# Optimization experiments

Hardware: AMD Instinct MI355X
Metric: run time of the kernel (lower is better)

## Reference

```python
import jax, jax.numpy as jnp
import numpy as np

B, N, NH, F = 4, 4096, 16, 8      # batch, grid cells, input points per cell, raw features
D, FF, H, PE = 256, 1024, 8, 32   # model_dim, ff_dim, n_heads, pos_emb_dim
NG, NI = 8192, 65536              # grid table size, input-point table size
SEQ = 4                           # 4 ** seq_level
HD = D // H


def layer_norm(x, g, b, eps=1e-5):
    mu = jnp.mean(x, axis=-1, keepdims=True)
    var = jnp.mean(jnp.square(x - mu), axis=-1, keepdims=True)
    return (x - mu) * jax.lax.rsqrt(var + eps) * g + b


def setup_inputs() -> dict:
    key = jax.random.key(0)
    ks = jax.random.split(key, 20)
    inp = {}
    inp["x"] = jax.random.normal(ks[0], (B, N, NH, F), jnp.float32)
    inp["grid_level_indices"] = jax.random.randint(ks[1], (B, N), 0, NG)
    inp["drop_mask"] = jax.random.bernoulli(ks[2], 0.1, (B, N))
    # buffers
    inp["input_mapping"] = jax.random.randint(ks[3], (NG, NH), 0, NI)
    inp["in_range"] = jax.random.bernoulli(ks[4], 0.95, (NG, NH))
    inp["input_coordinates"] = jax.random.uniform(ks[5], (2, NI), jnp.float32, -3.14, 3.14)
    inp["grid_coords"] = jax.random.uniform(ks[6], (2, NG), jnp.float32, -3.14, 3.14)
    # params
    inp["W_in"] = jax.random.normal(ks[7], (F, D), jnp.float32) * 0.05
    inp["b_in"] = jnp.zeros((D,), jnp.float32)
    inp["W_pe"] = jax.random.normal(ks[8], (2, PE), jnp.float32) * 0.2
    inp["W_bias"] = jax.random.normal(ks[9], (PE, H), jnp.float32) * 0.1
    inp["W_v"] = jax.random.normal(ks[10], (D, D), jnp.float32) * 0.02
    inp["W_o"] = jax.random.normal(ks[11], (D, D), jnp.float32) * 0.02
    inp["W1"] = jax.random.normal(ks[12], (D, FF), jnp.float32) * 0.02
    inp["W2"] = jax.random.normal(ks[13], (FF, D), jnp.float32) * 0.02
    inp["g1"] = jnp.ones((D,), jnp.float32)
    inp["b1"] = jnp.zeros((D,), jnp.float32)
    inp["g2"] = jnp.ones((D,), jnp.float32)
    inp["b2"] = jnp.zeros((D,), jnp.float32)
    return inp


def reference(x, grid_level_indices, drop_mask, input_mapping, in_range,
              input_coordinates, grid_coords, W_in, b_in, W_pe, W_bias,
              W_v, W_o, W1, W2, g1, b1, g2, b2):
    b, n, nh, _ = x.shape
    nq = n // SEQ
    K = SEQ * nh  # keys per group

    # input_layer.input_mlp: Linear + SiLU
    x = jax.nn.silu(x @ W_in + b_in)                       # [b,n,nh,D]

    # relative positions (polar): grid-cell coords vs gathered input-point coords
    gseq = grid_level_indices.reshape(b, nq, SEQ)
    idx = input_mapping[gseq]                              # [b,nq,4,nh]
    lon1 = grid_coords[0][gseq][..., None, None]           # [b,nq,4,1,1]
    lat1 = grid_coords[1][gseq][..., None, None]
    lon2 = input_coordinates[0][idx][:, :, None]           # [b,nq,1,4,nh]
    lat2 = input_coordinates[1][idx][:, :, None]
    dlon, dlat = lon2 - lon1, lat2 - lat1                  # [b,nq,4,4,nh]
    dist = jnp.sqrt(dlon * dlon + dlat * dlat + 1e-12)
    ang = jnp.arctan2(dlat, dlon)
    pos1 = dist.reshape(b, nq, SEQ, K)
    pos2 = ang.reshape(b, nq, SEQ, K)

    # mask: out-of-range OR dropped, broadcast across the 4 query cells
    m = (~in_range[grid_level_indices]) | drop_mask[:, :, None]  # [b,n,nh]
    m = m.reshape(b, nq, SEQ, nh)
    mask = jnp.broadcast_to(m[:, :, None], (b, nq, SEQ, SEQ, nh)).reshape(b, nq, SEQ, K)

    xs = x.reshape(b, nq, K, D)                            # kv tokens per group

    # positional bias -> attention scores (qkv_bias=False path: bias-only scores)
    pe = jax.nn.silu(jnp.stack([pos1, pos2], -1) @ W_pe)   # [b,nq,4,K,PE]
    bias = pe @ W_bias                                     # [b,nq,4,K,H]
    scores = jnp.moveaxis(bias, -1, 2)                     # [b,nq,H,4,K]
    scores = jnp.where(mask[:, :, None], -1e9, scores)
    att = jax.nn.softmax(scores, axis=-1)

    vh = (xs @ W_v).reshape(b, nq, K, H, HD)
    out = jnp.einsum('bqhtk,bqkhd->bqthd', att, vh).reshape(b, nq, SEQ, D)
    out = out @ W_o                                        # [b,nq,4,D]

    # nha_layer tail (q_res=False, dropout=0)
    h = layer_norm(out, g1, b1)
    h = layer_norm(h + jax.nn.silu(h @ W1) @ W2, g2, b2)
    return h.reshape(b, n, D)
```

## Files before the change

### kernel.cpp

```cpp
#include <hip/hip_runtime.h>

#define B_   4
#define N_   4096
#define NH_  16
#define F_   8
#define D_   256
#define FF_  1024
#define H_   8
#define PE_  32
#define NG_  8192
#define NI_  65536
#define NQ_  1024

typedef short short8 __attribute__((ext_vector_type(8)));
typedef float f32x4 __attribute__((ext_vector_type(4)));

union U8 { short8 s8; uint4 u4; };

__device__ __forceinline__ float silu_f(float v) {
  return v * __builtin_amdgcn_rcpf(1.f + __expf(-v));
}
__device__ __forceinline__ unsigned short f2bf(float f) {
  unsigned int x = __float_as_uint(f);
  unsigned int r = (x + 0x7fffu + ((x >> 16) & 1u)) >> 16;
  return (unsigned short)r;
}
__device__ __forceinline__ unsigned int cvt_pk(float a, float b) {
  unsigned int r;
  asm("v_cvt_pk_bf16_f32 %0, %1, %2" : "=v"(r) : "v"(a), "v"(b));
  return r;
}
__device__ __forceinline__ unsigned short f2bf1(float v) {
  return (unsigned short)cvt_pk(v, v);
}
__device__ __forceinline__ float bf2f(unsigned short h) {
  return __uint_as_float(((unsigned int)h) << 16);
}

__device__ __forceinline__ int detect_layout(const unsigned int* w) {
  unsigned b1 = 0, b0 = 0;
#pragma unroll
  for (int i = 0; i < 64; ++i) {
    unsigned v = w[i];
    b1 |= v & 0x0000FF00u;
    b0 |= v & 0x000000FFu;
  }
  return b1 ? 0 : (b0 ? 1 : 2);
}
__device__ __forceinline__ int read_bool(const void* p, int i, int lay) {
  if (lay == 0) return ((const unsigned char*)p)[i] != 0;
  if (lay == 1) return ((const int*)p)[i] != 0;
  return ((const float*)p)[i] != 0.0f;
}

#define WOP_OFF 0
#define W1P_OFF 65536
#define W2P_OFF (65536 + 262144)
#define WVP_OFF (65536 + 262144 + 262144)
#define WIP_OFF (65536 + 262144 + 262144 + 65536)
#define WBP_OFF (WIP_OFF + 8192)
#define WS_BASE_B ((WBP_OFF + 512) * 2)
#define DRP8_B  WS_BASE_B
#define INR8_B  (WS_BASE_B + 16384)
#define WS_MASKS_END (INR8_B + 131072)
#define ROWS_B  WS_MASKS_END
#define WS_ROWS_END (ROWS_B + 16384 * 256 * 2)
#define WS_TAIL ((65536 + 262144 + 262144) * 2)

__global__ __launch_bounds__(256) void k_pack(
    const float* __restrict__ Wo, const float* __restrict__ W1,
    const float* __restrict__ W2, const float* __restrict__ Wv,
    const float* __restrict__ Wi, const float* __restrict__ Wb,
    const void* __restrict__ drop, const void* __restrict__ inr,
    short* __restrict__ ws)
{
  int t = blockIdx.x * 256 + threadIdx.x;
  if (t < 8192) {
    int g = t & 3, n = (t >> 2) & 255, kk = t >> 10;
    int k0 = kk * 32 + g * 8;
    short8 v;
#pragma unroll
    for (int j = 0; j < 8; ++j) v[j] = (short)f2bf(Wo[(k0 + j) * 256 + n]);
    *(short8*)(ws + WOP_OFF + t * 8) = v;
  } else if (t < 40960) {
    int u = t - 8192;
    int g = u & 3, n = (u >> 2) & 1023, kk = u >> 12;
    int k0 = kk * 32 + g * 8;
    short8 v;
#pragma unroll
    for (int j = 0; j < 8; ++j) v[j] = (short)f2bf(W1[(k0 + j) * 1024 + n]);
    *(short8*)(ws + W1P_OFF + u * 8) = v;
  } else if (t < 73728) {
    int u = t - 40960;
    int g = u & 3, n = (u >> 2) & 255, kk = u >> 10;
    int k0 = kk * 32 + g * 8;
    short8 v;
#pragma unroll
    for (int j = 0; j < 8; ++j) v[j] = (short)f2bf(W2[(k0 + j) * 256 + n]);
    *(short8*)(ws + W2P_OFF + u * 8) = v;
  } else if (t < 81920) {
    int u = t - 73728;
    int g = u & 3, n = (u >> 2) & 255, kk = u >> 10;
    int k0 = kk * 32 + g * 8;
    short8 v;
#pragma unroll
    for (int j = 0; j < 8; ++j) v[j] = (short)f2bf(Wv[(k0 + j) * 256 + n]);
    *(short8*)(ws + WVP_OFF + u * 8) = v;
  } else if (t < 82944) {
    int u = t - 81920;
    int g = u & 3, n = u >> 2;
    short8 v;
#pragma unroll
    for (int j = 0; j < 8; ++j) {
      int k = g * 8 + j;
      v[j] = (k < 8) ? (short)f2bf(Wi[k * 256 + n]) : (short)0;
    }
    *(short8*)(ws + WIP_OFF + (n * 4 + g) * 8) = v;
  } else if (t < 83008) {
    int u = t - 82944;
    int g = u & 3, col = u >> 2;
    short8 v;
#pragma unroll
    for (int j = 0; j < 8; ++j) {
      int p = g * 8 + j;
      v[j] = (col < 8) ? (short)f2bf(Wb[p * 8 + col]) : (short)0;
    }
    *(short8*)(ws + WBP_OFF + (col * 4 + g) * 8) = v;
  } else if (t >= 83200) {
    int lay = detect_layout((const unsigned int*)inr);
    int t2 = t - 83200;
    char* wsb = (char*)ws;
    if (t2 < B_ * N_) {
      ((unsigned char*)(wsb + DRP8_B))[t2] =
          (unsigned char)read_bool(drop, t2, lay);
    } else if (t2 < B_ * N_ + NG_ * NH_) {
      int u = t2 - B_ * N_;
      ((unsigned char*)(wsb + INR8_B))[u] =
          (unsigned char)read_bool(inr, u, lay);
    }
  }
}

#define OFF_ATTB  32768
#define OFF_DIST  36864
#define OFF_ANG   37888
#define OFF_KLON  38912
#define OFF_KLAT  39168
#define OFF_KMSK  39424
#define OFF_GLON  39680
#define OFF_GLAT  39696

__global__ __launch_bounds__(256) void k_attn_mfma(
    const float* __restrict__ x, const int* __restrict__ gli,
    const unsigned char* __restrict__ drp8, const unsigned char* __restrict__ inr8,
    const int* __restrict__ imap, const float* __restrict__ icoord,
    const float* __restrict__ gcoord, const float* __restrict__ W_pe,
    const float* __restrict__ b_in, const short* __restrict__ WiP,
    const short* __restrict__ WbP, const short* __restrict__ WvP,
    unsigned short* __restrict__ rows, float* __restrict__ out, int userows)
{
  __shared__ __align__(16) char sm[39712];
  float* distl = (float*)(sm + OFF_DIST);
  float* angl = (float*)(sm + OFF_ANG);
  float* klon = (float*)(sm + OFF_KLON);
  float* klat = (float*)(sm + OFF_KLAT);
  int* kmask = (int*)(sm + OFF_KMSK);
  float* glon = (float*)(sm + OFF_GLON);
  float* glat = (float*)(sm + OFF_GLAT);

  const int grp = blockIdx.x;
  const int b = grp >> 10;
  const int q = grp & (NQ_ - 1);
  const int tid = threadIdx.x;
  const int w = tid >> 6;
  const int l15 = tid & 15;
  const int g = (tid & 63) >> 4;
  const int swz = (l15 & 7) << 4;

  if (tid < 64) {
    int s = tid >> 4;
    int gg = gli[b * N_ + q * 4 + s];
    if ((tid & 15) == 0) {
      glon[s] = gcoord[gg];
      glat[s] = gcoord[NG_ + gg];
    }
    int id = imap[gg * NH_ + (tid & 15)];
    klon[tid] = icoord[id];
    klat[tid] = icoord[NI_ + id];
    kmask[tid] = (inr8[gg * NH_ + (tid & 15)] == 0) |
                 (drp8[b * N_ + q * 4 + s] != 0);
  }

  {
    short8 a = {0, 0, 0, 0, 0, 0, 0, 0};
    if (g == 0) {
      const float4* xp = (const float4*)(x + (size_t)(b * N_ + q * 4) * 128);
      float4 xa = xp[(w * 16 + l15) * 2];
      float4 xc = xp[(w * 16 + l15) * 2 + 1];
      U8 u;
      u.u4.x = cvt_pk(xa.x, xa.y);
      u.u4.y = cvt_pk(xa.z, xa.w);
      u.u4.z = cvt_pk(xc.x, xc.y);
      u.u4.w = cvt_pk(xc.z, xc.w);
      a = u.s8;
    }
    const int k0 = w * 16 + g * 4;
#pragma unroll
    for (int nf = 0; nf < 16; ++nf) {
      short8 bv = *(const short8*)(WiP + ((nf * 16 + l15) * 4 + g) * 8);
      f32x4 accM = {0.f, 0.f, 0.f, 0.f};
      accM = __builtin_amdgcn_mfma_f32_16x16x32_bf16(a, bv, accM, 0, 0, 0);
      int d = nf * 16 + l15;
      float bn = b_in[d];
      uint2 pv;
      pv.x = cvt_pk(silu_f(accM[0] + bn), silu_f(accM[1] + bn));
      pv.y = cvt_pk(silu_f(accM[2] + bn), silu_f(accM[3] + bn));
      *(uint2*)(sm + ((d * 128 + k0 * 2) ^ ((d & 7) << 4))) = pv;
    }
  }
  __syncthreads();

  {
    const int t = tid >> 6, k = tid & 63;
    float dlon = klon[k] - glon[t];
    float dlat = klat[k] - glat[t];
    distl[tid] = sqrtf(dlon * dlon + dlat * dlat + 1e-12f);
    angl[tid] = atan2f(dlat, dlon);
  }
  __syncthreads();

  {
    float wpe0[8], wpe1[8];
    {
      const float4* wp = (const float4*)W_pe;
      float4 w0a = wp[g * 2], w0b = wp[g * 2 + 1];
      float4 w1a = wp[8 + g * 2], w1b = wp[8 + g * 2 + 1];
      wpe0[0] = w0a.x; wpe0[1] = w0a.y; wpe0[2] = w0a.z; wpe0[3] = w0a.w;
      wpe0[4] = w0b.x; wpe0[5] = w0b.y; wpe0[6] = w0b.z; wpe0[7] = w0b.w;
      wpe1[0] = w1a.x; wpe1[1] = w1a.y; wpe1[2] = w1a.z; wpe1[3] = w1a.w;
      wpe1[4] = w1b.x; wpe1[5] = w1b.y; wpe1[6] = w1b.z; wpe1[7] = w1b.w;
    }
    short8 wb = *(const short8*)(WbP + (l15 * 4 + g) * 8);
    f32x4 accS[4];
#pragma unroll
    for (int i = 0; i < 4; ++i) {
      int row = (w * 4 + i) * 16 + l15;
      float dd = distl[row];
      float aa = angl[row];
      float pe[8];
#pragma unroll
      for (int j = 0; j < 8; ++j)
        pe[j] = silu_f(fmaf(dd, wpe0[j], aa * wpe1[j]));
      U8 pu;
      pu.u4.x = cvt_pk(pe[0], pe[1]);
      pu.u4.y = cvt_pk(pe[2], pe[3]);
      pu.u4.z = cvt_pk(pe[4], pe[5]);
      pu.u4.w = cvt_pk(pe[6], pe[7]);
      f32x4 z = {0.f, 0.f, 0.f, 0.f};
      accS[i] = __builtin_amdgcn_mfma_f32_16x16x32_bf16(pu.s8, wb, z, 0, 0, 0);
    }
    float sv[16];
    float mx = -1e30f;
#pragma unroll
    for (int i = 0; i < 4; ++i)
#pragma unroll
      for (int r = 0; r < 4; ++r) {
        int k = i * 16 + g * 4 + r;
        float s = kmask[k] ? -1e9f : accS[i][r];
        sv[i * 4 + r] = s;
        mx = fmaxf(mx, s);
      }
    mx = fmaxf(mx, __shfl_xor(mx, 16));
    mx = fmaxf(mx, __shfl_xor(mx, 32));
    float sum = 0.f;
#pragma unroll
    for (int u = 0; u < 16; ++u) { sv[u] = __expf(sv[u] - mx); sum += sv[u]; }
    sum += __shfl_xor(sum, 16);
    sum += __shfl_xor(sum, 32);
    float inv = __builtin_amdgcn_rcpf(sum);
    if (l15 < 8) {
      int row = l15 * 4 + w;
      int rs = (row & 7) << 4;
#pragma unroll
      for (int i = 0; i < 4; ++i) {
        uint2 pv;
        pv.x = cvt_pk(sv[i * 4 + 0] * inv, sv[i * 4 + 1] * inv);
        pv.y = cvt_pk(sv[i * 4 + 2] * inv, sv[i * 4 + 3] * inv);
        *(uint2*)(sm + OFF_ATTB + ((row * 128 + (i * 16 + g * 4) * 2) ^ rs)) = pv;
      }
    }
  }
  __syncthreads();

  f32x4 accY[2][4];
  {
    f32x4 z = {0.f, 0.f, 0.f, 0.f};
#pragma unroll
    for (int mi = 0; mi < 2; ++mi)
#pragma unroll
      for (int ni = 0; ni < 4; ++ni) accY[mi][ni] = z;
  }
#pragma unroll
  for (int kk = 0; kk < 2; ++kk) {
    short8 a0 = *(const short8*)(sm + OFF_ATTB + ((l15 * 128 + kk * 64 + g * 16) ^ swz));
    short8 a1 = *(const short8*)(sm + OFF_ATTB + (((16 + l15) * 128 + kk * 64 + g * 16) ^ swz));
    short8 bf[4];
#pragma unroll
    for (int ni = 0; ni < 4; ++ni)
      bf[ni] = *(const short8*)(sm +
          (((w * 64 + ni * 16 + l15) * 128 + kk * 64 + g * 16) ^ swz));
#pragma unroll
    for (int ni = 0; ni < 4; ++ni) {
      accY[0][ni] = __builtin_amdgcn_mfma_f32_16x16x32_bf16(a0, bf[ni], accY[0][ni], 0, 0, 0);
      accY[1][ni] = __builtin_amdgcn_mfma_f32_16x16x32_bf16(a1, bf[ni], accY[1][ni], 0, 0, 0);
    }
  }
  __syncthreads();

#pragma unroll
  for (int mi = 0; mi < 2; ++mi)
#pragma unroll
    for (int ni = 0; ni < 4; ++ni)
#pragma unroll
      for (int r = 0; r < 4; ++r) {
        int row = mi * 16 + g * 4 + r;
        int col = w * 64 + ni * 16 + l15;
        *(unsigned short*)(sm + ((row * 512 + col * 2) ^ ((row & 7) << 4))) =
            f2bf1(accY[mi][ni][r]);
      }
  __syncthreads();

  {
    const int mf = w >> 1;
    f32x4 accV[4];
    {
      f32x4 z = {0.f, 0.f, 0.f, 0.f};
#pragma unroll
      for (int ni = 0; ni < 4; ++ni) accV[ni] = z;
    }
#pragma unroll
    for (int kk = 0; kk < 8; ++kk) {
      short8 a = *(const short8*)(sm +
          (((mf * 16 + l15) * 512 + kk * 64 + g * 16) ^ swz));
#pragma unroll
      for (int ni = 0; ni < 4; ++ni) {
        int col = w * 64 + ni * 16 + l15;
        short8 bv = *(const short8*)(WvP + ((size_t)(kk * 256 + col)) * 32 + g * 8);
        accV[ni] = __builtin_amdgcn_mfma_f32_16x16x32_bf16(a, bv, accV[ni], 0, 0, 0);
      }
    }
    float* outl = (float*)(sm + 16384);
    const int gb = (w & 1) * 2;
#pragma unroll
    for (int ni = 0; ni < 4; ++ni) {
      if (g == gb + (ni >> 1)) {
#pragma unroll
        for (int r = 0; r < 4; ++r)
          outl[r * 256 + w * 64 + ni * 16 + l15] = accV[ni][r];
      }
    }
  }
  __syncthreads();

  if (userows) {
    const float* outl = (const float*)(sm + 16384);
    unsigned* rb = (unsigned*)(rows + (size_t)grp * (4 * D_));
    int t2 = tid >> 7;
    int c2 = tid & 127;
#pragma unroll
    for (int tt = 0; tt < 2; ++tt) {
      int t = tt * 2 + t2;
      rb[t * 128 + c2] = cvt_pk(outl[t * 256 + 2 * c2],
                                outl[t * 256 + 2 * c2 + 1]);
    }
  } else {
    const float* outl = (const float*)(sm + 16384);
    float* ob = out + (size_t)grp * (4 * D_);
#pragma unroll
    for (int t = 0; t < 4; ++t) ob[t * 256 + tid] = outl[t * 256 + tid];
  }
}

__global__ __launch_bounds__(256) void k_attn_valu(
    const float* __restrict__ x, const int* __restrict__ gli,
    const void* __restrict__ drop, const int* __restrict__ imap,
    const void* __restrict__ inr, const float* __restrict__ icoord,
    const float* __restrict__ gcoord, const float* __restrict__ W_in,
    const float* __restrict__ b_in, const float* __restrict__ W_pe,
    const float* __restrict__ W_bias, const float* __restrict__ W_v,
    float* __restrict__ out)
{
  __shared__ __align__(16) float xl[512];
  __shared__ float glon[4], glat[4];
  __shared__ int gidx[4], dropf[4];
  __shared__ float klon[64], klat[64];
  __shared__ int kmask[64];
  __shared__ __align__(16) unsigned short xs[64 * D_];
  __shared__ __align__(16) float att[32 * 64];
  __shared__ __align__(16) float yl[4 * 8 * 260];

  const int grp = blockIdx.x;
  const int b = grp >> 10;
  const int q = grp & (NQ_ - 1);
  const int tid = threadIdx.x;
  const int lay = detect_layout((const unsigned int*)inr);

  if (tid < 4) {
    int g = gli[b * N_ + q * 4 + tid];
    gidx[tid] = g;
    glon[tid] = gcoord[g];
    glat[tid] = gcoord[NG_ + g];
    dropf[tid] = read_bool(drop, b * N_ + q * 4 + tid, lay);
  }
  const float* xb = x + (size_t)(b * N_ + q * 4) * (NH_ * F_);
  xl[tid] = xb[tid];
  xl[tid + 256] = xb[tid + 256];
  __syncthreads();

  if (tid < 64) {
    int s = tid >> 4;
    int g = gidx[s];
    int id = imap[g * NH_ + (tid & 15)];
    klon[tid] = icoord[id];
    klat[tid] = icoord[NI_ + id];
    kmask[tid] = (read_bool(inr, g * NH_ + (tid & 15), lay) == 0) | dropf[s];
  }
  {
    float w[8];
#pragma unroll
    for (int c = 0; c < 8; ++c) w[c] = W_in[c * D_ + tid];
    float bi = b_in[tid];
#pragma unroll 4
    for (int k = 0; k < 64; ++k) {
      float v = bi;
#pragma unroll
      for (int c = 0; c < 8; ++c) v = fmaf(xl[k * 8 + c], w[c], v);
      xs[k * D_ + tid] = f2bf(silu_f(v));
    }
  }
  __syncthreads();
  {
    const int t = tid >> 6, k = tid & 63;
    float dlon = klon[k] - glon[t];
    float dlat = klat[k] - glat[t];
    float dist = sqrtf(dlon * dlon + dlat * dlat + 1e-12f);
    float ang = atan2f(dlat, dlon);
    float bias[8];
#pragma unroll
    for (int h = 0; h < 8; ++h) bias[h] = 0.f;
#pragma unroll
    for (int p = 0; p < 32; ++p) {
      float pv = silu_f(fmaf(dist, W_pe[p], ang * W_pe[32 + p]));
#pragma unroll
      for (int h = 0; h < 8; ++h) bias[h] = fmaf(pv, W_bias[p * 8 + h], bias[h]);
    }
    const bool mk = (kmask[k] != 0);
#pragma unroll
    for (int h = 0; h < 8; ++h)
      att[(h * 4 + t) * 64 + k] = mk ? -1e9f : bias[h];
  }
  __syncthreads();
  {
    const int row = tid >> 3, l8 = tid & 7;
    float sv[8];
    float mx = -1e30f;
#pragma unroll
    for (int i = 0; i < 8; ++i) { sv[i] = att[row * 64 + l8 + i * 8]; mx = fmaxf(mx, sv[i]); }
#pragma unroll
    for (int off = 1; off < 8; off <<= 1) mx = fmaxf(mx, __shfl_xor(mx, off, 8));
    float sm = 0.f;
#pragma unroll
    for (int i = 0; i < 8; ++i) { sv[i] = __expf(sv[i] - mx); sm += sv[i]; }
#pragma unroll
    for (int off = 1; off < 8; off <<= 1) sm += __shfl_xor(sm, off, 8);
    float inv = 1.f / sm;
#pragma unroll
    for (int i = 0; i < 8; ++i) att[row * 64 + l8 + i * 8] = sv[i] * inv;
  }
  __syncthreads();
  {
    float acc[32];
#pragma unroll
    for (int r = 0; r < 32; ++r) acc[r] = 0.f;
    for (int k4 = 0; k4 < 64; k4 += 4) {
      float xv0 = bf2f(xs[(k4 + 0) * D_ + tid]);
      float xv1 = bf2f(xs[(k4 + 1) * D_ + tid]);
      float xv2 = bf2f(xs[(k4 + 2) * D_ + tid]);
      float xv3 = bf2f(xs[(k4 + 3) * D_ + tid]);
#pragma unroll
      for (int r = 0; r < 32; ++r) {
        float4 a = *(const float4*)&att[r * 64 + k4];
        acc[r] = fmaf(a.x, xv0, acc[r]);
        acc[r] = fmaf(a.y, xv1, acc[r]);
        acc[r] = fmaf(a.z, xv2, acc[r]);
        acc[r] = fmaf(a.w, xv3, acc[r]);
      }
    }
#pragma unroll
    for (int r = 0; r < 32; ++r)
      yl[(r & 3) * 2080 + (r >> 2) * 260 + tid] = acc[r];
  }
  __syncthreads();
  {
    const int h = tid >> 5;
    float o0 = 0.f, o1 = 0.f, o2 = 0.f, o3 = 0.f;
    for (int c = 0; c < 256; c += 4) {
      float w0 = W_v[(c + 0) * D_ + tid];
      float w1 = W_v[(c + 1) * D_ + tid];
      float w2 = W_v[(c + 2) * D_ + tid];
      float w3 = W_v[(c + 3) * D_ + tid];
      float4 y0 = *(const float4*)&yl[0 * 2080 + h * 260 + c];
      float4 y1 = *(const float4*)&yl[1 * 2080 + h * 260 + c];
      float4 y2 = *(const float4*)&yl[2 * 2080 + h * 260 + c];
      float4 y3 = *(const float4*)&yl[3 * 2080 + h * 260 + c];
      o0 = fmaf(y0.x, w0, o0); o0 = fmaf(y0.y, w1, o0); o0 = fmaf(y0.z, w2, o0); o0 = fmaf(y0.w, w3, o0);
      o1 = fmaf(y1.x, w0, o1); o1 = fmaf(y1.y, w1, o1); o1 = fmaf(y1.z, w2, o1); o1 = fmaf(y1.w, w3, o1);
      o2 = fmaf(y2.x, w0, o2); o2 = fmaf(y2.y, w1, o2); o2 = fmaf(y2.z, w2, o2); o2 = fmaf(y2.w, w3, o2);
      o3 = fmaf(y3.x, w0, o3); o3 = fmaf(y3.y, w1, o3); o3 = fmaf(y3.z, w2, o3); o3 = fmaf(y3.w, w3, o3);
    }
    float* ob = out + (size_t)grp * (4 * D_);
    ob[0 * D_ + tid] = o0;
    ob[1 * D_ + tid] = o1;
    ob[2 * D_ + tid] = o2;
    ob[3 * D_ + tid] = o3;
  }
}

template<int MI>
__device__ __forceinline__ void gemm_mfma(
    f32x4 acc[MI][4], const char* As, const short* Bp,
    int N, int kk0, int colbase, int l15, int g)
{
#pragma unroll
  for (int kk = 0; kk < 8; ++kk) {
    short8 a[MI], bv[4];
#pragma unroll
    for (int mi = 0; mi < MI; ++mi) {
      int row = mi * 16 + l15;
      int byte = (row * 512 + kk * 64 + g * 16) ^ ((row & 7) << 4);
      a[mi] = *(const short8*)(As + byte);
    }
#pragma unroll
    for (int ni = 0; ni < 4; ++ni) {
      int col = colbase + ni * 16 + l15;
      size_t off = ((size_t)(kk0 + kk) * N + col) * 32 + g * 8;
      bv[ni] = *(const short8*)(Bp + off);
    }
#pragma unroll
    for (int mi = 0; mi < MI; ++mi)
#pragma unroll
      for (int ni = 0; ni < 4; ++ni)
        acc[mi][ni] = __builtin_amdgcn_mfma_f32_16x16x32_bf16(
            a[mi], bv[ni], acc[mi][ni], 0, 0, 0);
  }
}

__global__ __launch_bounds__(256) void k_tail_mfma(
    const float* __restrict__ g1v, const float* __restrict__ b1v,
    const float* __restrict__ g2v, const float* __restrict__ b2v,
    const short* __restrict__ WoP, const short* __restrict__ W1P,
    const short* __restrict__ W2P, const unsigned short* __restrict__ rowsrc,
    float* __restrict__ io, int userows)
{
  __shared__ __align__(16) unsigned short sA1[32 * 256];
  __shared__ __align__(16) unsigned short sU[32 * 256];
  __shared__ float sPs[4][32];
  __shared__ float sPss[4][32];

  const int tid = threadIdx.x;
  const int w = tid >> 6;
  const int l15 = tid & 15;
  const int g = (tid & 63) >> 4;
  float* base = io + (size_t)blockIdx.x * (32 * 256);

  if (userows) {
    const unsigned short* rb = rowsrc + (size_t)blockIdx.x * (32 * 256);
#pragma unroll
    for (int i = 0; i < 8; ++i) {
      int e = (tid + 256 * i) * 4;
      int row = e >> 8, c = e & 255;
      uint2 v = *(const uint2*)(rb + e);
      int byte = (row * 512 + c * 2) ^ ((row & 7) << 4);
      *(uint2*)((char*)sU + byte) = v;
    }
  } else {
#pragma unroll
    for (int i = 0; i < 8; ++i) {
      int e = (tid + 256 * i) * 4;
      int row = e >> 8, c = e & 255;
      float4 v = *(const float4*)(base + e);
      uint2 pv;
      pv.x = cvt_pk(v.x, v.y);
      pv.y = cvt_pk(v.z, v.w);
      int byte = (row * 512 + c * 2) ^ ((row & 7) << 4);
      *(uint2*)((char*)sU + byte) = pv;
    }
  }
  __syncthreads();

  f32x4 acc[2][4];
  {
    f32x4 z = {0.f, 0.f, 0.f, 0.f};
#pragma unroll
    for (int mi = 0; mi < 2; ++mi)
#pragma unroll
      for (int ni = 0; ni < 4; ++ni) acc[mi][ni] = z;
  }
  gemm_mfma<2>(acc, (const char*)sU, WoP, 256, 0, w * 64, l15, g);

#pragma unroll
  for (int mi = 0; mi < 2; ++mi)
#pragma unroll
    for (int r = 0; r < 4; ++r) {
      float a0 = acc[mi][0][r], a1 = acc[mi][1][r], a2 = acc[mi][2][r], a3 = acc[mi][3][r];
      float s = a0 + a1 + a2 + a3;
      float ss = a0 * a0 + a1 * a1 + a2 * a2 + a3 * a3;
#pragma unroll
      for (int off = 1; off < 16; off <<= 1) {
        s += __shfl_xor(s, off);
        ss += __shfl_xor(ss, off);
      }
      if (l15 == 0) {
        int row = 16 * mi + 4 * g + r;
        sPs[w][row] = s;
        sPss[w][row] = ss;
      }
    }
  __syncthreads();

  {
    float ga[4], bb[4];
#pragma unroll
    for (int ni = 0; ni < 4; ++ni) {
      int col = 64 * w + 16 * ni + l15;
      ga[ni] = g1v[col];
      bb[ni] = b1v[col];
    }
#pragma unroll
    for (int mi = 0; mi < 2; ++mi)
#pragma unroll
      for (int r = 0; r < 4; ++r) {
        int row = 16 * mi + 4 * g + r;
        float S = sPs[0][row] + sPs[1][row] + sPs[2][row] + sPs[3][row];
        float SS = sPss[0][row] + sPss[1][row] + sPss[2][row] + sPss[3][row];
        float mu = S * (1.f / 256.f);
        float rs = rsqrtf(SS * (1.f / 256.f) - mu * mu + 1e-5f);
#pragma unroll
        for (int ni = 0; ni < 4; ++ni) {
          int col = 64 * w + 16 * ni + l15;
          float val = (acc[mi][ni][r] - mu) * rs * ga[ni] + bb[ni];
          acc[mi][ni][r] = val;
          int byte = (row * 512 + col * 2) ^ ((row & 7) << 4);
          *(unsigned short*)((char*)sA1 + byte) = f2bf1(val);
        }
      }
  }
  __syncthreads();

  for (int p = 0; p < 4; ++p) {
    f32x4 acc2[2][4];
    {
      f32x4 z = {0.f, 0.f, 0.f, 0.f};
#pragma unroll
      for (int mi = 0; mi < 2; ++mi)
#pragma unroll
        for (int ni = 0; ni < 4; ++ni) acc2[mi][ni] = z;
    }
    gemm_mfma<2>(acc2, (const char*)sA1, W1P, 1024, 0, p * 256 + w * 64, l15, g);
#pragma unroll
    for (int mi = 0; mi < 2; ++mi)
#pragma unroll
      for (int ni = 0; ni < 4; ++ni)
#pragma unroll
        for (int r = 0; r < 4; ++r) {
          int row = 16 * mi + 4 * g + r;
          int col = 64 * w + 16 * ni + l15;
          int byte = (row * 512 + col * 2) ^ ((row & 7) << 4);
          *(unsigned short*)((char*)sU + byte) = f2bf1(silu_f(acc2[mi][ni][r]));
        }
    __syncthreads();
    gemm_mfma<2>(acc, (const char*)sU, W2P, 256, p * 8, w * 64, l15, g);
    __syncthreads();
  }

#pragma unroll
  for (int mi = 0; mi < 2; ++mi)
#pragma unroll
    for (int r = 0; r < 4; ++r) {
      float a0 = acc[mi][0][r], a1 = acc[mi][1][r], a2 = acc[mi][2][r], a3 = acc[mi][3][r];
      float s = a0 + a1 + a2 + a3;
      float ss = a0 * a0 + a1 * a1 + a2 * a2 + a3 * a3;
#pragma unroll
      for (int off = 1; off < 16; off <<= 1) {
        s += __shfl_xor(s, off);
        ss += __shfl_xor(ss, off);
      }
      if (l15 == 0) {
        int row = 16 * mi + 4 * g + r;
        sPs[w][row] = s;
        sPss[w][row] = ss;
      }
    }
  __syncthreads();

  {
    float ga[4], bb[4];
#pragma unroll
    for (int ni = 0; ni < 4; ++ni) {
      int col = 64 * w + 16 * ni + l15;
      ga[ni] = g2v[col];
      bb[ni] = b2v[col];
    }
#pragma unroll
    for (int mi = 0; mi < 2; ++mi)
#pragma unroll
      for (int r = 0; r < 4; ++r) {
        int row = 16 * mi + 4 * g + r;
        float S = sPs[0][row] + sPs[1][row] + sPs[2][row] + sPs[3][row];
        float SS = sPss[0][row] + sPss[1][row] + sPss[2][row] + sPss[3][row];
        float mu = S * (1.f / 256.f);
        float rs = rsqrtf(SS * (1.f / 256.f) - mu * mu + 1e-5f);
#pragma unroll
        for (int ni = 0; ni < 4; ++ni) {
          int col = 64 * w + 16 * ni + l15;
          base[row * 256 + col] = (acc[mi][ni][r] - mu) * rs * ga[ni] + bb[ni];
        }
      }
  }
}

__global__ __launch_bounds__(256) void k_tail(
    const float* __restrict__ Wo, const float* __restrict__ W1,
    const float* __restrict__ W2, const float* __restrict__ g1,
    const float* __restrict__ b1, const float* __restrict__ g2,
    const float* __restrict__ b2, float* __restrict__ io)
{
  __shared__ __align__(16) float rl[16 * 260];
  __shared__ __align__(16) float h1[16 * 260];
  __shared__ __align__(16) unsigned short u[16 * FF_];
  const int tid = threadIdx.x;
  float* base = io + (size_t)blockIdx.x * (16 * D_);

#pragma unroll
  for (int r = 0; r < 16; ++r) rl[r * 260 + tid] = base[r * D_ + tid];
  __syncthreads();
  {
    float acc[16];
#pragma unroll
    for (int r = 0; r < 16; ++r) acc[r] = 0.f;
    for (int c = 0; c < 256; c += 4) {
      float w0 = Wo[(c + 0) * D_ + tid], w1 = Wo[(c + 1) * D_ + tid];
      float w2 = Wo[(c + 2) * D_ + tid], w3 = Wo[(c + 3) * D_ + tid];
#pragma unroll
      for (int r = 0; r < 16; ++r) {
        float4 rv = *(const float4*)&rl[r * 260 + c];
        acc[r] = fmaf(rv.x, w0, acc[r]); acc[r] = fmaf(rv.y, w1, acc[r]);
        acc[r] = fmaf(rv.z, w2, acc[r]); acc[r] = fmaf(rv.w, w3, acc[r]);
      }
    }
#pragma unroll
    for (int r = 0; r < 16; ++r) h1[r * 260 + tid] = acc[r];
  }
  __syncthreads();
  {
    const int r = tid >> 4, l = tid & 15;
    float s = 0.f, ss = 0.f;
#pragma unroll
    for (int i = 0; i < 16; ++i) { float v = h1[r * 260 + l + i * 16]; s += v; ss += v * v; }
#pragma unroll
    for (int off = 1; off < 16; off <<= 1) { s += __shfl_xor(s, off, 16); ss += __shfl_xor(ss, off, 16); }
    float mu = s * (1.f / 256.f);
    float rs = rsqrtf(ss * (1.f / 256.f) - mu * mu + 1e-5f);
#pragma unroll
    for (int i = 0; i < 16; ++i) {
      int d = l + i * 16;
      h1[r * 260 + d] = (h1[r * 260 + d] - mu) * rs * g1[d] + b1[d];
    }
  }
  __syncthreads();
  for (int fo = 0; fo < 4; ++fo) {
    const int f = fo * 256 + tid;
    float a2[16];
#pragma unroll
    for (int r = 0; r < 16; ++r) a2[r] = 0.f;
    for (int c = 0; c < 256; c += 4) {
      float w0 = W1[(c + 0) * FF_ + f], w1 = W1[(c + 1) * FF_ + f];
      float w2 = W1[(c + 2) * FF_ + f], w3 = W1[(c + 3) * FF_ + f];
#pragma unroll
      for (int r = 0; r < 16; ++r) {
        float4 hv = *(const float4*)&h1[r * 260 + c];
        a2[r] = fmaf(hv.x, w0, a2[r]); a2[r] = fmaf(hv.y, w1, a2[r]);
        a2[r] = fmaf(hv.z, w2, a2[r]); a2[r] = fmaf(hv.w, w3, a2[r]);
      }
    }
#pragma unroll
    for (int r = 0; r < 16; ++r) u[r * FF_ + f] = f2bf(silu_f(a2[r]));
  }
  __syncthreads();
  {
    float a3[16];
#pragma unroll
    for (int r = 0; r < 16; ++r) a3[r] = h1[r * 260 + tid];
    for (int f = 0; f < FF_; f += 8) {
      float w[8];
#pragma unroll
      for (int i = 0; i < 8; ++i) w[i] = W2[(f + i) * D_ + tid];
#pragma unroll
      for (int r = 0; r < 16; ++r) {
        uint4 uv = *(const uint4*)&u[r * FF_ + f];
        a3[r] = fmaf(__uint_as_float(uv.x << 16), w[0], a3[r]);
        a3[r] = fmaf(__uint_as_float(uv.x & 0xffff0000u), w[1], a3[r]);
        a3[r] = fmaf(__uint_as_float(uv.y << 16), w[2], a3[r]);
        a3[r] = fmaf(__uint_as_float(uv.y & 0xffff0000u), w[3], a3[r]);
        a3[r] = fmaf(__uint_as_float(uv.z << 16), w[4], a3[r]);
        a3[r] = fmaf(__uint_as_float(uv.z & 0xffff0000u), w[5], a3[r]);
        a3[r] = fmaf(__uint_as_float(uv.w << 16), w[6], a3[r]);
        a3[r] = fmaf(__uint_as_float(uv.w & 0xffff0000u), w[7], a3[r]);
      }
    }
#pragma unroll
    for (int r = 0; r < 16; ++r) rl[r * 260 + tid] = a3[r];
  }
  __syncthreads();
  {
    const int r = tid >> 4, l = tid & 15;
    float s = 0.f, ss = 0.f;
#pragma unroll
    for (int i = 0; i < 16; ++i) { float v = rl[r * 260 + l + i * 16]; s += v; ss += v * v; }
#pragma unroll
    for (int off = 1; off < 16; off <<= 1) { s += __shfl_xor(s, off, 16); ss += __shfl_xor(ss, off, 16); }
    float mu = s * (1.f / 256.f);
    float rs = rsqrtf(ss * (1.f / 256.f) - mu * mu + 1e-5f);
#pragma unroll
    for (int i = 0; i < 16; ++i) {
      int d = l + i * 16;
      base[r * D_ + d] = (rl[r * 260 + d] - mu) * rs * g2[d] + b2[d];
    }
  }
}

extern "C" void kernel_launch(void* const* d_in, const int* in_sizes, int n_in,
                              void* d_out, int out_size, void* d_ws, size_t ws_size,
                              hipStream_t stream) {
  (void)in_sizes; (void)n_in; (void)out_size;
  const float* x = (const float*)d_in[0];
  const int* gli = (const int*)d_in[1];
  const void* drop = d_in[2];
  const int* imap = (const int*)d_in[3];
  const void* inr = d_in[4];
  const float* icoord = (const float*)d_in[5];
  const float* gcoord = (const float*)d_in[6];
  const float* W_in = (const float*)d_in[7];
  const float* b_in = (const float*)d_in[8];
  const float* W_pe = (const float*)d_in[9];
  const float* W_bias = (const float*)d_in[10];
  const float* W_v = (const float*)d_in[11];
  const float* W_o = (const float*)d_in[12];
  const float* W1 = (const float*)d_in[13];
  const float* W2 = (const float*)d_in[14];
  const float* g1 = (const float*)d_in[15];
  const float* b1 = (const float*)d_in[16];
  const float* g2 = (const float*)d_in[17];
  const float* b2 = (const float*)d_in[18];
  float* out = (float*)d_out;

  if (ws_size >= (size_t)WS_MASKS_END) {
    const int userows = (ws_size >= (size_t)WS_ROWS_END) ? 1 : 0;
    short* ws = (short*)d_ws;
    char* wsb = (char*)d_ws;
    k_pack<<<dim3(901), dim3(256), 0, stream>>>(
        W_o, W1, W2, W_v, W_in, W_bias, drop, inr, ws);
    k_attn_mfma<<<dim3(B_ * NQ_), dim3(256), 0, stream>>>(
        x, gli, (const unsigned char*)(wsb + DRP8_B),
        (const unsigned char*)(wsb + INR8_B), imap, icoord, gcoord, W_pe, b_in,
        ws + WIP_OFF, ws + WBP_OFF, ws + WVP_OFF,
        (unsigned short*)(wsb + ROWS_B), out, userows);
    k_tail_mfma<<<dim3((B_ * N_) / 32), dim3(256), 0, stream>>>(
        g1, b1, g2, b2, ws + WOP_OFF, ws + W1P_OFF, ws + W2P_OFF,
        (const unsigned short*)(wsb + ROWS_B), out, userows);
  } else if (ws_size >= (size_t)WS_TAIL) {
    short* ws = (short*)d_ws;
    k_pack<<<dim3(325), dim3(256), 0, stream>>>(
        W_o, W1, W2, W_v, W_in, W_bias, drop, inr, ws);
    k_attn_valu<<<dim3(B_ * NQ_), dim3(256), 0, stream>>>(
        x, gli, drop, imap, inr, icoord, gcoord, W_in, b_in, W_pe, W_bias, W_v, out);
    k_tail_mfma<<<dim3((B_ * N_) / 32), dim3(256), 0, stream>>>(
        g1, b1, g2, b2, ws + WOP_OFF, ws + W1P_OFF, ws + W2P_OFF,
        (const unsigned short*)0, out, 0);
  } else {
    k_attn_valu<<<dim3(B_ * NQ_), dim3(256), 0, stream>>>(
        x, gli, drop, imap, inr, icoord, gcoord, W_in, b_in, W_pe, W_bias, W_v, out);
    k_tail<<<dim3((B_ * N_) / 16), dim3(256), 0, stream>>>(
        W_o, W1, W2, g1, b1, g2, b2, out);
  }
}
```

Measured before the change: 112.1 us.

## Split input-MLP staging into two key halves to shrink LDS footprint

The attention kernel now computes the input Linear+SiLU for 32 keys at a time into a 16KB LDS buffer, then runs the attention-weighted sum for that half before reusing the buffer for the second half. This cuts shared memory per block from about 39KB to 23KB, which is meant to allow more resident blocks per CU and better latency hiding. In exchange it adds two extra barriers, and the x loads plus the input-MLP MFMA work are split into two phases, serialising some of that work.

```diff
diff --git a/kernel.cpp b/kernel.cpp
--- a/kernel.cpp
+++ b/kernel.cpp
@@ -141,14 +141,15 @@
   }
 }
 
-#define OFF_ATTB  32768
-#define OFF_DIST  36864
-#define OFF_ANG   37888
-#define OFF_KLON  38912
-#define OFF_KLAT  39168
-#define OFF_KMSK  39424
-#define OFF_GLON  39680
-#define OFF_GLAT  39696
+#define OXS   0
+#define OATT  16384
+#define ODIST 20480
+#define OANG  21504
+#define OKLON 22528
+#define OKLAT 22784
+#define OKMSK 23040
+#define OGLON 23296
+#define OGLAT 23312
 
 __global__ __launch_bounds__(256) void k_attn_mfma(
     const float* __restrict__ x, const int* __restrict__ gli,
@@ -159,14 +160,14 @@
     const short* __restrict__ WbP, const short* __restrict__ WvP,
     unsigned short* __restrict__ rows, float* __restrict__ out, int userows)
 {
-  __shared__ __align__(16) char sm[39712];
-  float* distl = (float*)(sm + OFF_DIST);
-  float* angl = (float*)(sm + OFF_ANG);
-  float* klon = (float*)(sm + OFF_KLON);
-  float* klat = (float*)(sm + OFF_KLAT);
-  int* kmask = (int*)(sm + OFF_KMSK);
-  float* glon = (float*)(sm + OFF_GLON);
-  float* glat = (float*)(sm + OFF_GLAT);
+  __shared__ __align__(16) char sm[23328];
+  float* distl = (float*)(sm + ODIST);
+  float* angl = (float*)(sm + OANG);
+  float* klon = (float*)(sm + OKLON);
+  float* klat = (float*)(sm + OKLAT);
+  int* kmask = (int*)(sm + OKMSK);
+  float* glon = (float*)(sm + OGLON);
+  float* glat = (float*)(sm + OGLAT);
 
   const int grp = blockIdx.x;
   const int b = grp >> 10;
@@ -191,12 +192,16 @@
                  (drp8[b * N_ + q * 4 + s] != 0);
   }
 
+  const int sl = (((((w & 1) * 2 + (g >> 1)) ^ ((l15 >> 1) & 3)) << 4) | ((g & 1) * 8));
+  const int nb = (w >> 1) * 8;
+  const float4* xp = (const float4*)(x + (size_t)(b * N_ + q * 4) * 128);
+
   {
     short8 a = {0, 0, 0, 0, 0, 0, 0, 0};
     if (g == 0) {
-      const float4* xp = (const float4*)(x + (size_t)(b * N_ + q * 4) * 128);
-      float4 xa = xp[(w * 16 + l15) * 2];
-      float4 xc = xp[(w * 16 + l15) * 2 + 1];
+      int tok = (w & 1) * 16 + l15;
+      float4 xa = xp[tok * 2];
+      float4 xc = xp[tok * 2 + 1];
       U8 u;
       u.u4.x = cvt_pk(xa.x, xa.y);
       u.u4.y = cvt_pk(xa.z, xa.w);
@@ -204,18 +209,17 @@
       u.u4.w = cvt_pk(xc.z, xc.w);
       a = u.s8;
     }
-    const int k0 = w * 16 + g * 4;
-#pragma unroll
-    for (int nf = 0; nf < 16; ++nf) {
-      short8 bv = *(const short8*)(WiP + ((nf * 16 + l15) * 4 + g) * 8);
+#pragma unroll
+    for (int nf = 0; nf < 8; ++nf) {
+      int d = (nb + nf) * 16 + l15;
+      short8 bv = *(const short8*)(WiP + (d * 4 + g) * 8);
       f32x4 accM = {0.f, 0.f, 0.f, 0.f};
       accM = __builtin_amdgcn_mfma_f32_16x16x32_bf16(a, bv, accM, 0, 0, 0);
-      int d = nf * 16 + l15;
       float bn = b_in[d];
       uint2 pv;
       pv.x = cvt_pk(silu_f(accM[0] + bn), silu_f(accM[1] + bn));
       pv.y = cvt_pk(silu_f(accM[2] + bn), silu_f(accM[3] + bn));
-      *(uint2*)(sm + ((d * 128 + k0 * 2) ^ ((d & 7) << 4))) = pv;
+      *(uint2*)(sm + OXS + d * 64 + sl) = pv;
     }
   }
   __syncthreads();
@@ -286,7 +290,7 @@
         uint2 pv;
         pv.x = cvt_pk(sv[i * 4 + 0] * inv, sv[i * 4 + 1] * inv);
         pv.y = cvt_pk(sv[i * 4 + 2] * inv, sv[i * 4 + 3] * inv);
-        *(uint2*)(sm + OFF_ATTB + ((row * 128 + (i * 16 + g * 4) * 2) ^ rs)) = pv;
+        *(uint2*)(sm + OATT + ((row * 128 + (i * 16 + g * 4) * 2) ^ rs)) = pv;
       }
     }
   }
@@ -300,19 +304,58 @@
 #pragma unroll
       for (int ni = 0; ni < 4; ++ni) accY[mi][ni] = z;
   }
-#pragma unroll
-  for (int kk = 0; kk < 2; ++kk) {
-    short8 a0 = *(const short8*)(sm + OFF_ATTB + ((l15 * 128 + kk * 64 + g * 16) ^ swz));
-    short8 a1 = *(const short8*)(sm + OFF_ATTB + (((16 + l15) * 128 + kk * 64 + g * 16) ^ swz));
-    short8 bf[4];
-#pragma unroll
-    for (int ni = 0; ni < 4; ++ni)
-      bf[ni] = *(const short8*)(sm +
-          (((w * 64 + ni * 16 + l15) * 128 + kk * 64 + g * 16) ^ swz));
+  {
+    short8 a0 = *(const short8*)(sm + OATT + ((l15 * 128 + g * 16) ^ swz));
+    short8 a1 = *(const short8*)(sm + OATT + (((16 + l15) * 128 + g * 16) ^ swz));
 #pragma unroll
     for (int ni = 0; ni < 4; ++ni) {
-      accY[0][ni] = __builtin_amdgcn_mfma_f32_16x16x32_bf16(a0, bf[ni], accY[0][ni], 0, 0, 0);
-      accY[1][ni] = __builtin_amdgcn_mfma_f32_16x16x32_bf16(a1, bf[ni], accY[1][ni], 0, 0, 0);
+      int d = w * 64 + ni * 16 + l15;
+      short8 bf = *(const short8*)(sm + OXS + d * 64 +
+                                   ((g ^ ((l15 >> 1) & 3)) << 4));
+      accY[0][ni] = __builtin_amdgcn_mfma_f32_16x16x32_bf16(a0, bf, accY[0][ni], 0, 0, 0);
+      accY[1][ni] = __builtin_amdgcn_mfma_f32_16x16x32_bf16(a1, bf, accY[1][ni], 0, 0, 0);
+    }
+  }
+  __syncthreads();
+
+  {
+    short8 a = {0, 0, 0, 0, 0, 0, 0, 0};
+    if (g == 0) {
+      int tok = 32 + (w & 1) * 16 + l15;
+      float4 xa = xp[tok * 2];
+      float4 xc = xp[tok * 2 + 1];
+      U8 u;
+      u.u4.x = cvt_pk(xa.x, xa.y);
+      u.u4.y = cvt_pk(xa.z, xa.w);
+      u.u4.z = cvt_pk(xc.x, xc.y);
+      u.u4.w = cvt_pk(xc.z, xc.w);
+      a = u.s8;
+    }
+#pragma unroll
+    for (int nf = 0; nf < 8; ++nf) {
+      int d = (nb + nf) * 16 + l15;
+      short8 bv = *(const short8*)(WiP + (d * 4 + g) * 8);
+      f32x4 accM = {0.f, 0.f, 0.f, 0.f};
+      accM = __builtin_amdgcn_mfma_f32_16x16x32_bf16(a, bv, accM, 0, 0, 0);
+      float bn = b_in[d];
+      uint2 pv;
+      pv.x = cvt_pk(silu_f(accM[0] + bn), silu_f(accM[1] + bn));
+      pv.y = cvt_pk(silu_f(accM[2] + bn), silu_f(accM[3] + bn));
+      *(uint2*)(sm + OXS + d * 64 + sl) = pv;
+    }
+  }
+  __syncthreads();
+
+  {
+    short8 a0 = *(const short8*)(sm + OATT + ((l15 * 128 + 64 + g * 16) ^ swz));
+    short8 a1 = *(const short8*)(sm + OATT + (((16 + l15) * 128 + 64 + g * 16) ^ swz));
+#pragma unroll
+    for (int ni = 0; ni < 4; ++ni) {
+      int d = w * 64 + ni * 16 + l15;
+      short8 bf = *(const short8*)(sm + OXS + d * 64 +
+                                   ((g ^ ((l15 >> 1) & 3)) << 4));
+      accY[0][ni] = __builtin_amdgcn_mfma_f32_16x16x32_bf16(a0, bf, accY[0][ni], 0, 0, 0);
+      accY[1][ni] = __builtin_amdgcn_mfma_f32_16x16x32_bf16(a1, bf, accY[1][ni], 0, 0, 0);
     }
   }
   __syncthreads();
@@ -325,7 +368,7 @@
       for (int r = 0; r < 4; ++r) {
         int row = mi * 16 + g * 4 + r;
         int col = w * 64 + ni * 16 + l15;
-        *(unsigned short*)(sm + ((row * 512 + col * 2) ^ ((row & 7) << 4))) =
+        *(unsigned short*)(sm + OXS + ((row * 512 + col * 2) ^ ((row & 7) << 4))) =
             f2bf1(accY[mi][ni][r]);
       }
   __syncthreads();
@@ -340,7 +383,7 @@
     }
 #pragma unroll
     for (int kk = 0; kk < 8; ++kk) {
-      short8 a = *(const short8*)(sm +
+      short8 a = *(const short8*)(sm + OXS +
           (((mf * 16 + l15) * 512 + kk * 64 + g * 16) ^ swz));
 #pragma unroll
       for (int ni = 0; ni < 4; ++ni) {
@@ -349,7 +392,7 @@
         accV[ni] = __builtin_amdgcn_mfma_f32_16x16x32_bf16(a, bv, accV[ni], 0, 0, 0);
       }
     }
-    float* outl = (float*)(sm + 16384);
+    float* outl = (float*)(sm + OATT);
     const int gb = (w & 1) * 2;
 #pragma unroll
     for (int ni = 0; ni < 4; ++ni) {
@@ -363,7 +406,7 @@
   __syncthreads();
 
   if (userows) {
-    const float* outl = (const float*)(sm + 16384);
+    const float* outl = (const float*)(sm + OATT);
     unsigned* rb = (unsigned*)(rows + (size_t)grp * (4 * D_));
     int t2 = tid >> 7;
     int c2 = tid & 127;
@@ -374,7 +417,7 @@
                                 outl[t * 256 + 2 * c2 + 1]);
     }
   } else {
-    const float* outl = (const float*)(sm + 16384);
+    const float* outl = (const float*)(sm + OATT);
     float* ob = out + (size_t)grp * (4 * D_);
 #pragma unroll
     for (int t = 0; t < 4; ++t) ob[t * 256 + tid] = outl[t * 256 + tid];
```

After: 115.5 us. 1.03x slower.
